# Performance work log

Hardware: AMD Instinct MI355X
Metric: run time of the kernel (lower is better)

## Reference

```python
import jax, jax.numpy as jnp
import numpy as np

N_NODES = 100000
N_EDGES = 1600000
N_GRAPHS = 256
IN_DIM, HID_DIM, FC_DIM, OUT_DIM = 205, 128, 64, 2


def _gcn_conv(x, W, b, src, dst, n):
    # PyG GCNConv: linear transform, add self-loops, symmetric normalization,
    # scatter-add aggregation.  x: [N, Fin] -> [N, Fout]
    h = x @ W  # [N, Fout]
    deg = jnp.zeros((n,), dtype=h.dtype).at[dst].add(1.0) + 1.0  # in-degree + self-loop
    dinv_sqrt = jax.lax.rsqrt(deg)
    norm = dinv_sqrt[src] * dinv_sqrt[dst]  # [E]
    msgs = h[src] * norm[:, None]  # gather + scale, [E, Fout]
    agg = jax.ops.segment_sum(msgs, dst, num_segments=n)
    agg = agg + h * (1.0 / deg)[:, None]  # self-loop contribution (dinv_sqrt[i]^2)
    return agg + b


def _mean_pool(x, batch, g):
    sums = jax.ops.segment_sum(x, batch, num_segments=g)
    counts = jax.ops.segment_sum(jnp.ones((x.shape[0],), dtype=x.dtype), batch, num_segments=g)
    return sums / jnp.maximum(counts, 1.0)[:, None]


def setup_inputs() -> dict:
    key = jax.random.key(0)
    ks = jax.random.split(key, 10)
    x = jax.random.normal(ks[0], (N_NODES, IN_DIM), dtype=jnp.float32)
    edge_index = jax.random.randint(ks[1], (2, N_EDGES), 0, N_NODES, dtype=jnp.int64)
    batch = jnp.sort(jax.random.randint(ks[2], (N_NODES,), 0, N_GRAPHS, dtype=jnp.int64))

    def glorot(k, shape):
        lim = float(np.sqrt(6.0 / (shape[0] + shape[1])))
        return jax.random.uniform(k, shape, jnp.float32, -lim, lim)

    return {
        "x": x,
        "edge_index": edge_index,
        "batch": batch,
        "W1": glorot(ks[3], (IN_DIM, HID_DIM)),
        "b1": jnp.zeros((HID_DIM,), jnp.float32),
        "W2": glorot(ks[4], (HID_DIM, HID_DIM)),
        "b2": jnp.zeros((HID_DIM,), jnp.float32),
        "Wf1": glorot(ks[5], (HID_DIM, FC_DIM)),
        "bf1": jnp.zeros((FC_DIM,), jnp.float32),
        "Wf2": glorot(ks[6], (FC_DIM, OUT_DIM)),
        "bf2": jnp.zeros((OUT_DIM,), jnp.float32),
    }


def reference(x, edge_index, batch, W1, b1, W2, b2, Wf1, bf1, Wf2, bf2):
    src, dst = edge_index[0], edge_index[1]
    n = x.shape[0]
    h = jax.nn.relu(_gcn_conv(x, W1, b1, src, dst, n))  # dropout is identity in eval
    h = jax.nn.relu(_gcn_conv(h, W2, b2, src, dst, n))
    g = _mean_pool(h, batch, N_GRAPHS)  # [G, HID]
    g = jax.nn.relu(g @ Wf1 + bf1)
    return g @ Wf2 + bf2  # [G, OUT]
```

## Files before the change

kernel.cpp:

```cpp
#include <hip/hip_runtime.h>
#include <hip/hip_bf16.h>


#define N_NODES 100000
#define N_EDGES 1600000
#define N_GRAPHS 256
#define IN_DIM 205
#define HID 128
#define FC_DIM 64
#define OUT_DIM 2


__global__ void k_count(const int* __restrict__ dst, int* __restrict__ cnt, int e) {
    int i = blockIdx.x * blockDim.x + threadIdx.x;
    if (i < e) atomicAdd(&cnt[dst[i]], 1);
}

__global__ void k_deg(const int* __restrict__ cnt, float* __restrict__ dinv, int n) {
    int i = blockIdx.x * blockDim.x + threadIdx.x;
    if (i < n) {
        float deg = (float)cnt[i] + 1.0f;
        dinv[i] = rsqrtf(deg);
    }
}

__global__ __launch_bounds__(256) void k_scan1(const int* __restrict__ cnt,
                                               int* __restrict__ row,
                                               int* __restrict__ bsum, int n) {
    __shared__ int s[256];
    int t = threadIdx.x;
    int i = blockIdx.x * 256 + t;
    int v = (i < n) ? cnt[i] : 0;
    s[t] = v;
    __syncthreads();
    for (int off = 1; off < 256; off <<= 1) {
        int add = (t >= off) ? s[t - off] : 0;
        __syncthreads();
        s[t] += add;
        __syncthreads();
    }
    if (i < n) row[i] = s[t] - v;
    if (t == 255) bsum[blockIdx.x] = s[255];
}

__global__ __launch_bounds__(512) void k_scan2(int* __restrict__ bsum,
                                               int* __restrict__ boff, int nb) {
    __shared__ int s[512];
    int t = threadIdx.x;
    int v = (t < nb) ? bsum[t] : 0;
    s[t] = v;
    __syncthreads();
    for (int off = 1; off < 512; off <<= 1) {
        int add = (t >= off) ? s[t - off] : 0;
        __syncthreads();
        s[t] += add;
        __syncthreads();
    }
    if (t < nb) boff[t] = s[t] - v;
}

__global__ void k_scan3b(int* __restrict__ row, const int* __restrict__ boff,
                         int* __restrict__ cursor, int n, int e) {
    int i = blockIdx.x * blockDim.x + threadIdx.x;
    if (i < n) {
        int r = row[i] + boff[i >> 8];
        row[i] = r;
        cursor[i] = r;
    }
    if (i == 0) row[n] = e;
}

__global__ void k_fill(const int* __restrict__ src, const int* __restrict__ dst,
                       int* __restrict__ cursor, int* __restrict__ col, int e) {
    int i = blockIdx.x * blockDim.x + threadIdx.x;
    if (i < e) {
        int d = dst[i];
        int pos = atomicAdd(&cursor[d], 1);
        col[pos] = src[i];
    }
}


#define BM 128
#define BK 32

template <bool VEC4A>
__global__ __launch_bounds__(256) void k_gemm(const float* __restrict__ A,
                                              const float* __restrict__ W,
                                              const float* __restrict__ dinv,
                                              float* __restrict__ C, int n, int K) {
    __shared__ float As[BK][BM + 4];
    __shared__ float Ws[BK][HID];
    int tid = threadIdx.x;
    int tx = tid & 15;
    int ty = tid >> 4;
    int rowBase = blockIdx.x * BM;

    float acc[8][8];
#pragma unroll
    for (int i = 0; i < 8; ++i)
#pragma unroll
        for (int j = 0; j < 8; ++j) acc[i][j] = 0.f;

    for (int k0 = 0; k0 < K; k0 += BK) {
        {
            int r = tid >> 1;
            int kg = (tid & 1) * 16;
            int grow = rowBase + r;
            if (VEC4A) {
                float4 a[4];
#pragma unroll
                for (int u = 0; u < 4; ++u) a[u] = make_float4(0.f, 0.f, 0.f, 0.f);
                if (grow < n) {
                    const float* ap = &A[(size_t)grow * K + k0 + kg];
#pragma unroll
                    for (int u = 0; u < 4; ++u) a[u] = *(const float4*)(ap + u * 4);
                }
#pragma unroll
                for (int u = 0; u < 4; ++u) {
                    As[kg + u * 4 + 0][r] = a[u].x;
                    As[kg + u * 4 + 1][r] = a[u].y;
                    As[kg + u * 4 + 2][r] = a[u].z;
                    As[kg + u * 4 + 3][r] = a[u].w;
                }
            } else {
#pragma unroll
                for (int u = 0; u < 16; ++u) {
                    int kk = k0 + kg + u;
                    float v = 0.f;
                    if (grow < n && kk < K) v = A[(size_t)grow * K + kk];
                    As[kg + u][r] = v;
                }
            }
        }
        {
            int kk = tid >> 3;
            int cg = (tid & 7) * 16;
            int gk = k0 + kk;
#pragma unroll
            for (int u = 0; u < 4; ++u) {
                float4 v = make_float4(0.f, 0.f, 0.f, 0.f);
                if (gk < K) v = *(const float4*)&W[(size_t)gk * HID + cg + u * 4];
                *(float4*)&Ws[kk][cg + u * 4] = v;
            }
        }
        __syncthreads();
#pragma unroll
        for (int k = 0; k < BK; ++k) {
            float4 a0 = *(const float4*)&As[k][ty * 8];
            float4 a1 = *(const float4*)&As[k][ty * 8 + 4];
            float4 w0 = *(const float4*)&Ws[k][tx * 4];
            float4 w1 = *(const float4*)&Ws[k][64 + tx * 4];
            float av[8] = {a0.x, a0.y, a0.z, a0.w, a1.x, a1.y, a1.z, a1.w};
            float wv[8] = {w0.x, w0.y, w0.z, w0.w, w1.x, w1.y, w1.z, w1.w};
#pragma unroll
            for (int i = 0; i < 8; ++i)
#pragma unroll
                for (int j = 0; j < 8; ++j) acc[i][j] = fmaf(av[i], wv[j], acc[i][j]);
        }
        __syncthreads();
    }
#pragma unroll
    for (int i = 0; i < 8; ++i) {
        int grow = rowBase + ty * 8 + i;
        if (grow < n) {
            float d = dinv[grow];
            float4 o0 = make_float4(d * acc[i][0], d * acc[i][1], d * acc[i][2], d * acc[i][3]);
            float4 o1 = make_float4(d * acc[i][4], d * acc[i][5], d * acc[i][6], d * acc[i][7]);
            *(float4*)&C[(size_t)grow * HID + tx * 4] = o0;
            *(float4*)&C[(size_t)grow * HID + 64 + tx * 4] = o1;
        }
    }
}


__global__ __launch_bounds__(256) void k_agg(const float* __restrict__ hs,
                                             const int* __restrict__ rowp,
                                             const int* __restrict__ col,
                                             const float* __restrict__ dinv,
                                             const float* __restrict__ bias,
                                             float* __restrict__ out, int n) {
    int wid = (blockIdx.x * blockDim.x + threadIdx.x) >> 6;
    int lane = threadIdx.x & 63;
    if (wid >= n) return;
    int beg = rowp[wid];
    int end = rowp[wid + 1];
    const float2* h2 = (const float2*)hs;
    float2 self = h2[(size_t)wid * 64 + lane];
    float ax = self.x, ay = self.y;
    int e = beg;
    for (; e + 4 <= end; e += 4) {
        int s0 = col[e], s1 = col[e + 1], s2 = col[e + 2], s3 = col[e + 3];
        float2 v0 = h2[(size_t)s0 * 64 + lane];
        float2 v1 = h2[(size_t)s1 * 64 + lane];
        float2 v2 = h2[(size_t)s2 * 64 + lane];
        float2 v3 = h2[(size_t)s3 * 64 + lane];
        ax += (v0.x + v1.x) + (v2.x + v3.x);
        ay += (v0.y + v1.y) + (v2.y + v3.y);
    }
    for (; e < end; ++e) {
        int s = col[e];
        float2 v = h2[(size_t)s * 64 + lane];
        ax += v.x;
        ay += v.y;
    }
    float2 bb = ((const float2*)bias)[lane];
    float di = dinv[wid];
    float ox = fmaf(di, ax, bb.x);
    float oy = fmaf(di, ay, bb.y);
    float2 o = make_float2(fmaxf(ox, 0.f), fmaxf(oy, 0.f));
    ((float2*)out)[(size_t)wid * 64 + lane] = o;
}


__global__ __launch_bounds__(256) void k_bounds(const int* __restrict__ batch,
                                                int* __restrict__ gstart, int n) {
    int g = threadIdx.x;
    int lo = 0, hi = n;
    while (lo < hi) {
        int mid = (lo + hi) >> 1;
        if (batch[mid] < g) lo = mid + 1; else hi = mid;
    }
    gstart[g] = lo;
    if (g == 0) gstart[N_GRAPHS] = n;
}

__global__ __launch_bounds__(256) void k_pool(const float* __restrict__ h,
                                              const int* __restrict__ gstart,
                                              float* __restrict__ gmean) {
    int g = blockIdx.x;
    int t = threadIdx.x;
    int f = t & 127;
    int half = t >> 7;
    int s = gstart[g], e = gstart[g + 1];
    float acc = 0.f;
    for (int r = s + half; r < e; r += 2) acc += h[(size_t)r * HID + f];
    __shared__ float red[256];
    red[t] = acc;
    __syncthreads();
    if (t < 128) {
        int cnt = e - s;
        float m = (red[t] + red[t + 128]) / (float)max(cnt, 1);
        gmean[(size_t)g * HID + t] = m;
    }
}


__global__ __launch_bounds__(64) void k_head(const float* __restrict__ gmean,
                                             const float* __restrict__ Wf1,
                                             const float* __restrict__ bf1,
                                             const float* __restrict__ Wf2,
                                             const float* __restrict__ bf2,
                                             float* __restrict__ out) {
    int g = blockIdx.x;
    int t = threadIdx.x;
    __shared__ float m[HID];
    __shared__ float a[FC_DIM];
    m[t] = gmean[(size_t)g * HID + t];
    m[t + 64] = gmean[(size_t)g * HID + t + 64];
    __syncthreads();
    float acc = bf1[t];
#pragma unroll 8
    for (int k = 0; k < HID; ++k) acc = fmaf(m[k], Wf1[k * FC_DIM + t], acc);
    a[t] = fmaxf(acc, 0.f);
    __syncthreads();
    if (t < OUT_DIM) {
        float o = bf2[t];
#pragma unroll 8
        for (int k = 0; k < FC_DIM; ++k) o = fmaf(a[k], Wf2[k * OUT_DIM + t], o);
        out[g * OUT_DIM + t] = o;
    }
}


extern "C" void kernel_launch(void* const* d_in, const int* in_sizes, int n_in,
                              void* d_out, int out_size, void* d_ws, size_t ws_size,
                              hipStream_t stream) {
    const float* x = (const float*)d_in[0];
    const int* ei = (const int*)d_in[1];
    const int* batch = (const int*)d_in[2];
    const float* W1 = (const float*)d_in[3];
    const float* b1 = (const float*)d_in[4];
    const float* W2 = (const float*)d_in[5];
    const float* b2 = (const float*)d_in[6];
    const float* Wf1 = (const float*)d_in[7];
    const float* bf1 = (const float*)d_in[8];
    const float* Wf2 = (const float*)d_in[9];
    const float* bf2 = (const float*)d_in[10];
    float* out = (float*)d_out;

    const int N = N_NODES, E = N_EDGES;
    const int* src = ei;
    const int* dst = ei + E;

    char* ws = (char*)d_ws;
    size_t off = 0;
    auto carve = [&](size_t bytes) -> char* {
        char* p = ws + off;
        off += (bytes + 255) & ~(size_t)255;
        return p;
    };
    float* t0 = (float*)carve((size_t)N * HID * 4);
    float* t1 = (float*)carve((size_t)N * HID * 4);
    int* cnt = (int*)carve((size_t)N * 4);
    int* rowp = (int*)carve((size_t)(N + 1) * 4);
    int* cursor = (int*)carve((size_t)N * 4);
    float* dinv = (float*)carve((size_t)N * 4);
    int* col = (int*)carve((size_t)E * 4);
    int* bsum = (int*)carve(4096);
    int* boff = (int*)carve(4096);
    int* gstart = (int*)carve((size_t)(N_GRAPHS + 1) * 4);
    float* gmean = (float*)carve((size_t)N_GRAPHS * HID * 4);
    (void)ws_size;

    hipMemsetAsync(cnt, 0, (size_t)N * 4, stream);

    const int TB = 256;
    int ebl = (E + TB - 1) / TB;
    int nbl = (N + TB - 1) / TB;

    k_count<<<ebl, TB, 0, stream>>>(dst, cnt, E);
    k_deg<<<nbl, TB, 0, stream>>>(cnt, dinv, N);
    int nscan = (N + 255) / 256;
    k_scan1<<<nscan, 256, 0, stream>>>(cnt, rowp, bsum, N);
    k_scan2<<<1, 512, 0, stream>>>(bsum, boff, nscan);
    k_scan3b<<<nscan, 256, 0, stream>>>(rowp, boff, cursor, N, E);
    k_fill<<<ebl, TB, 0, stream>>>(src, dst, cursor, col, E);

    int gblk = (N + BM - 1) / BM;
    k_gemm<false><<<gblk, 256, 0, stream>>>(x, W1, dinv, t0, N, IN_DIM);
    k_agg<<<(N * 64 + TB - 1) / TB, TB, 0, stream>>>(t0, rowp, col, dinv, b1, t1, N);

    k_gemm<true><<<gblk, 256, 0, stream>>>(t1, W2, dinv, t0, N, HID);
    k_agg<<<(N * 64 + TB - 1) / TB, TB, 0, stream>>>(t0, rowp, col, dinv, b2, t1, N);

    k_bounds<<<1, 256, 0, stream>>>(batch, gstart, N);
    k_pool<<<N_GRAPHS, 256, 0, stream>>>(t1, gstart, gmean);
    k_head<<<N_GRAPHS, 64, 0, stream>>>(gmean, Wf1, bf1, Wf2, bf2, out);
}
```

Baseline: 839.3 us.

## Use bf16x3 split MFMA for node feature GEMMs instead of FP32 FMA

Both dense GEMMs move from scalar FP32 FMA tiling onto MFMA 16x16x32 bf16 instructions. Each operand is split into high and low bf16 parts and three MFMA products are accumulated to keep near-FP32 accuracy. The weights are pre-split and transposed by a small per-call kernel, and the A tile is converted in registers before being staged in LDS. This targets the compute cost of the FP32 GEMMs, paid for with extra conversion work, more LDS traffic and non-vectorized scalar output stores.

Result: faster. 732.6 us (-12.7%).

```diff
diff --git a/kernel.cpp b/kernel.cpp
--- a/kernel.cpp
+++ b/kernel.cpp
@@ -9,6 +9,17 @@
 #define HID 128
 #define FC_DIM 64
 #define OUT_DIM 2
+#define KPAD1 224
+
+typedef float f32x4 __attribute__((ext_vector_type(4)));
+typedef short s16x8 __attribute__((ext_vector_type(8)));
+
+__device__ __forceinline__ ushort f2bf(float x) {
+    uint u = __float_as_uint(x);
+    u += 0x7fffu + ((u >> 16) & 1u);
+    return (ushort)(u >> 16);
+}
+__device__ __forceinline__ float bf2f(ushort b) { return __uint_as_float((uint)b << 16); }
 
 
 __global__ void k_count(const int* __restrict__ dst, int* __restrict__ cnt, int e) {
@@ -81,94 +92,138 @@
 }
 
 
-#define BM 128
-#define BK 32
+__global__ __launch_bounds__(256) void k_splitW(const float* __restrict__ W,
+                                                ushort* __restrict__ Wh,
+                                                ushort* __restrict__ Wl,
+                                                int K, int Kpad) {
+    int col = blockIdx.x;
+    int k = threadIdx.x;
+    if (k >= Kpad) return;
+    float a = (k < K) ? W[(size_t)k * HID + col] : 0.f;
+    ushort h = f2bf(a);
+    ushort l = f2bf(a - bf2f(h));
+    Wh[(size_t)col * Kpad + k] = h;
+    Wl[(size_t)col * Kpad + k] = l;
+}
+
 
 template <bool VEC4A>
-__global__ __launch_bounds__(256) void k_gemm(const float* __restrict__ A,
-                                              const float* __restrict__ W,
-                                              const float* __restrict__ dinv,
-                                              float* __restrict__ C, int n, int K) {
-    __shared__ float As[BK][BM + 4];
-    __shared__ float Ws[BK][HID];
+__global__ __launch_bounds__(256) void k_gemm_mfma(const float* __restrict__ A,
+                                                   const ushort* __restrict__ Wh,
+                                                   const ushort* __restrict__ Wl,
+                                                   const float* __restrict__ dinv,
+                                                   float* __restrict__ C,
+                                                   int n, int K, int Kpad) {
+    __shared__ ushort Ah[128 * 40];
+    __shared__ ushort Al[128 * 40];
+    __shared__ ushort Bh[128 * 40];
+    __shared__ ushort Bl[128 * 40];
+
     int tid = threadIdx.x;
-    int tx = tid & 15;
-    int ty = tid >> 4;
-    int rowBase = blockIdx.x * BM;
-
-    float acc[8][8];
-#pragma unroll
-    for (int i = 0; i < 8; ++i)
-#pragma unroll
-        for (int j = 0; j < 8; ++j) acc[i][j] = 0.f;
-
-    for (int k0 = 0; k0 < K; k0 += BK) {
-        {
-            int r = tid >> 1;
-            int kg = (tid & 1) * 16;
-            int grow = rowBase + r;
-            if (VEC4A) {
-                float4 a[4];
-#pragma unroll
-                for (int u = 0; u < 4; ++u) a[u] = make_float4(0.f, 0.f, 0.f, 0.f);
-                if (grow < n) {
-                    const float* ap = &A[(size_t)grow * K + k0 + kg];
-#pragma unroll
-                    for (int u = 0; u < 4; ++u) a[u] = *(const float4*)(ap + u * 4);
-                }
+    int lane = tid & 63;
+    int wave = tid >> 6;
+    int wy = wave >> 1;
+    int wx = wave & 1;
+    int r15 = lane & 15;
+    int g = lane >> 4;
+    int rowBase = blockIdx.x * 128;
+
+    f32x4 acc[4][4];
+#pragma unroll
+    for (int i = 0; i < 4; ++i)
+#pragma unroll
+        for (int j = 0; j < 4; ++j) acc[i][j] = (f32x4)(0.f);
+
+    int srow = tid >> 1;
+    int khalf = tid & 1;
+
+    for (int k0 = 0; k0 < Kpad; k0 += 32) {
+        float av[16];
+        int grow = rowBase + srow;
+        int kb = k0 + khalf * 16;
+        if (VEC4A) {
+            if (grow < n) {
+                const float* ap = &A[(size_t)grow * K + kb];
 #pragma unroll
                 for (int u = 0; u < 4; ++u) {
-                    As[kg + u * 4 + 0][r] = a[u].x;
-                    As[kg + u * 4 + 1][r] = a[u].y;
-                    As[kg + u * 4 + 2][r] = a[u].z;
-                    As[kg + u * 4 + 3][r] = a[u].w;
+                    float4 v = *(const float4*)(ap + 4 * u);
+                    av[4 * u + 0] = v.x; av[4 * u + 1] = v.y;
+                    av[4 * u + 2] = v.z; av[4 * u + 3] = v.w;
                 }
             } else {
 #pragma unroll
-                for (int u = 0; u < 16; ++u) {
-                    int kk = k0 + kg + u;
-                    float v = 0.f;
-                    if (grow < n && kk < K) v = A[(size_t)grow * K + kk];
-                    As[kg + u][r] = v;
+                for (int u = 0; u < 16; ++u) av[u] = 0.f;
+            }
+        } else {
+#pragma unroll
+            for (int u = 0; u < 16; ++u) {
+                int kk = kb + u;
+                av[u] = (grow < n && kk < K) ? A[(size_t)grow * K + kk] : 0.f;
+            }
+        }
+        uint hp[8], lp[8];
+#pragma unroll
+        for (int u = 0; u < 8; ++u) {
+            ushort h0 = f2bf(av[2 * u]), h1 = f2bf(av[2 * u + 1]);
+            ushort l0 = f2bf(av[2 * u] - bf2f(h0));
+            ushort l1 = f2bf(av[2 * u + 1] - bf2f(h1));
+            hp[u] = (uint)h0 | ((uint)h1 << 16);
+            lp[u] = (uint)l0 | ((uint)l1 << 16);
+        }
+        {
+            int base = srow * 40 + khalf * 16;
+            *(uint4*)&Ah[base]     = make_uint4(hp[0], hp[1], hp[2], hp[3]);
+            *(uint4*)&Ah[base + 8] = make_uint4(hp[4], hp[5], hp[6], hp[7]);
+            *(uint4*)&Al[base]     = make_uint4(lp[0], lp[1], lp[2], lp[3]);
+            *(uint4*)&Al[base + 8] = make_uint4(lp[4], lp[5], lp[6], lp[7]);
+        }
+        {
+            int col = srow;
+            size_t gofs = (size_t)col * Kpad + k0 + khalf * 16;
+            uint4 w0 = *(const uint4*)&Wh[gofs];
+            uint4 w1 = *(const uint4*)&Wh[gofs + 8];
+            uint4 x0 = *(const uint4*)&Wl[gofs];
+            uint4 x1 = *(const uint4*)&Wl[gofs + 8];
+            int wb = col * 40 + khalf * 16;
+            *(uint4*)&Bh[wb]     = w0;
+            *(uint4*)&Bh[wb + 8] = w1;
+            *(uint4*)&Bl[wb]     = x0;
+            *(uint4*)&Bl[wb + 8] = x1;
+        }
+        __syncthreads();
+        s16x8 afh[4], afl[4];
+#pragma unroll
+        for (int tr = 0; tr < 4; ++tr) {
+            int ai = (wy * 64 + tr * 16 + r15) * 40 + g * 8;
+            afh[tr] = *(const s16x8*)&Ah[ai];
+            afl[tr] = *(const s16x8*)&Al[ai];
+        }
+#pragma unroll
+        for (int tc = 0; tc < 4; ++tc) {
+            int bi = (wx * 64 + tc * 16 + r15) * 40 + g * 8;
+            s16x8 bfh = *(const s16x8*)&Bh[bi];
+            s16x8 bfl = *(const s16x8*)&Bl[bi];
+#pragma unroll
+            for (int tr = 0; tr < 4; ++tr) {
+                acc[tr][tc] = __builtin_amdgcn_mfma_f32_16x16x32_bf16(afh[tr], bfh, acc[tr][tc], 0, 0, 0);
+                acc[tr][tc] = __builtin_amdgcn_mfma_f32_16x16x32_bf16(afh[tr], bfl, acc[tr][tc], 0, 0, 0);
+                acc[tr][tc] = __builtin_amdgcn_mfma_f32_16x16x32_bf16(afl[tr], bfh, acc[tr][tc], 0, 0, 0);
+            }
+        }
+        __syncthreads();
+    }
+#pragma unroll
+    for (int tr = 0; tr < 4; ++tr) {
+#pragma unroll
+        for (int j = 0; j < 4; ++j) {
+            int grow = rowBase + wy * 64 + tr * 16 + g * 4 + j;
+            if (grow < n) {
+                float d = dinv[grow];
+#pragma unroll
+                for (int tc = 0; tc < 4; ++tc) {
+                    C[(size_t)grow * HID + wx * 64 + tc * 16 + r15] = d * acc[tr][tc][j];
                 }
             }
-        }
-        {
-            int kk = tid >> 3;
-            int cg = (tid & 7) * 16;
-            int gk = k0 + kk;
-#pragma unroll
-            for (int u = 0; u < 4; ++u) {
-                float4 v = make_float4(0.f, 0.f, 0.f, 0.f);
-                if (gk < K) v = *(const float4*)&W[(size_t)gk * HID + cg + u * 4];
-                *(float4*)&Ws[kk][cg + u * 4] = v;
-            }
-        }
-        __syncthreads();
-#pragma unroll
-        for (int k = 0; k < BK; ++k) {
-            float4 a0 = *(const float4*)&As[k][ty * 8];
-            float4 a1 = *(const float4*)&As[k][ty * 8 + 4];
-            float4 w0 = *(const float4*)&Ws[k][tx * 4];
-            float4 w1 = *(const float4*)&Ws[k][64 + tx * 4];
-            float av[8] = {a0.x, a0.y, a0.z, a0.w, a1.x, a1.y, a1.z, a1.w};
-            float wv[8] = {w0.x, w0.y, w0.z, w0.w, w1.x, w1.y, w1.z, w1.w};
-#pragma unroll
-            for (int i = 0; i < 8; ++i)
-#pragma unroll
-                for (int j = 0; j < 8; ++j) acc[i][j] = fmaf(av[i], wv[j], acc[i][j]);
-        }
-        __syncthreads();
-    }
-#pragma unroll
-    for (int i = 0; i < 8; ++i) {
-        int grow = rowBase + ty * 8 + i;
-        if (grow < n) {
-            float d = dinv[grow];
-            float4 o0 = make_float4(d * acc[i][0], d * acc[i][1], d * acc[i][2], d * acc[i][3]);
-            float4 o1 = make_float4(d * acc[i][4], d * acc[i][5], d * acc[i][6], d * acc[i][7]);
-            *(float4*)&C[(size_t)grow * HID + tx * 4] = o0;
-            *(float4*)&C[(size_t)grow * HID + 64 + tx * 4] = o1;
         }
     }
 }
@@ -311,6 +366,10 @@
     int* boff = (int*)carve(4096);
     int* gstart = (int*)carve((size_t)(N_GRAPHS + 1) * 4);
     float* gmean = (float*)carve((size_t)N_GRAPHS * HID * 4);
+    ushort* Wh1 = (ushort*)carve((size_t)HID * KPAD1 * 2);
+    ushort* Wl1 = (ushort*)carve((size_t)HID * KPAD1 * 2);
+    ushort* Wh2 = (ushort*)carve((size_t)HID * HID * 2);
+    ushort* Wl2 = (ushort*)carve((size_t)HID * HID * 2);
     (void)ws_size;
 
     hipMemsetAsync(cnt, 0, (size_t)N * 4, stream);
@@ -318,6 +377,9 @@
     const int TB = 256;
     int ebl = (E + TB - 1) / TB;
     int nbl = (N + TB - 1) / TB;
+
+    k_splitW<<<HID, 256, 0, stream>>>(W1, Wh1, Wl1, IN_DIM, KPAD1);
+    k_splitW<<<HID, 256, 0, stream>>>(W2, Wh2, Wl2, HID, HID);
 
     k_count<<<ebl, TB, 0, stream>>>(dst, cnt, E);
     k_deg<<<nbl, TB, 0, stream>>>(cnt, dinv, N);
@@ -327,11 +389,11 @@
     k_scan3b<<<nscan, 256, 0, stream>>>(rowp, boff, cursor, N, E);
     k_fill<<<ebl, TB, 0, stream>>>(src, dst, cursor, col, E);
 
-    int gblk = (N + BM - 1) / BM;
-    k_gemm<false><<<gblk, 256, 0, stream>>>(x, W1, dinv, t0, N, IN_DIM);
+    int gblk = (N + 127) / 128;
+    k_gemm_mfma<false><<<gblk, 256, 0, stream>>>(x, Wh1, Wl1, dinv, t0, N, IN_DIM, KPAD1);
     k_agg<<<(N * 64 + TB - 1) / TB, TB, 0, stream>>>(t0, rowp, col, dinv, b1, t1, N);
 
-    k_gemm<true><<<gblk, 256, 0, stream>>>(t1, W2, dinv, t0, N, HID);
+    k_gemm_mfma<true><<<gblk, 256, 0, stream>>>(t1, Wh2, Wl2, dinv, t0, N, HID, HID);
     k_agg<<<(N * 64 + TB - 1) / TB, TB, 0, stream>>>(t0, rowp, col, dinv, b2, t1, N);
 
     k_bounds<<<1, 256, 0, stream>>>(batch, gstart, N);
```
